# Optimization experiments

Hardware: AMD Instinct MI355X
Metric: run time of the kernel (lower is better)

The kernel has to match this reference:

```python
import jax, jax.numpy as jnp
import numpy as np

N = 100000   # nodes
E = 640000   # edges
D = 128      # in_channels
C = 40       # out_channels (classes)


def setup_inputs() -> dict:
    key = jax.random.key(0)
    ks = jax.random.split(key, 6)
    x = jax.random.normal(ks[0], (N, D), jnp.float32)
    edge_index = jax.random.randint(ks[1], (2, E), 0, N)
    edge_weight = jax.random.uniform(ks[2], (E,), jnp.float32)
    # 8 block convs (4 blocks x 2) stacked, + final conv
    Wb = jax.random.normal(ks[3], (8, D, D), jnp.float32) / np.sqrt(D)
    bb = jnp.zeros((8, D), jnp.float32)
    Wf = jax.random.normal(ks[4], (D, C), jnp.float32) / np.sqrt(D)
    bf = jnp.zeros((C,), jnp.float32)
    return dict(x=x, edge_index=edge_index, edge_weight=edge_weight,
                Wb=Wb, bb=bb, Wf=Wf, bf=bf)


def _gcn(x, W, b, src, dst, w):
    """PyG GCNConv (normalize=True) with self-loops already appended to src/dst/w."""
    n = x.shape[0]
    h = x @ W                                   # [N, out]
    deg = jax.ops.segment_sum(w, dst, num_segments=n)
    dinv = jnp.where(deg > 0, jax.lax.rsqrt(deg), 0.0)
    norm = dinv[src] * w * dinv[dst]            # [E+N]
    out = jax.ops.segment_sum(h[src] * norm[:, None], dst, num_segments=n)
    return out + b


def reference(x, edge_index, edge_weight, Wb, bb, Wf, bf):
    n = x.shape[0]
    loop = jnp.arange(n)
    src = jnp.concatenate([edge_index[0], loop])
    dst = jnp.concatenate([edge_index[1], loop])
    w = jnp.concatenate([edge_weight, jnp.ones((n,), x.dtype)])
    # forward only runs blocks 1-4 (blocks 5-7 unused in the original forward)
    for i in range(4):
        identity = x
        x = jax.nn.relu(_gcn(x, Wb[2 * i], bb[2 * i], src, dst, w))
        # dropout: identity in eval mode
        x = jax.nn.relu(_gcn(x, Wb[2 * i + 1], bb[2 * i + 1], src, dst, w))
        # F.normalize: row-wise L2 with eps=1e-12
        x = x / jnp.maximum(jnp.linalg.norm(x, axis=1, keepdims=True), 1e-12)
        x = (x + identity) / 2
    x = _gcn(x, Wf, bf, src, dst, w)
    return jax.nn.log_softmax(x, axis=1)
```

## Files before the change

kernel.cpp:

```cpp
#include <hip/hip_runtime.h>
#include <math.h>

#define NN 100000
#define EE 640000
#define DD 128
#define CC 40
#define FIXS 4194304.0f

typedef __bf16 bf16x8 __attribute__((ext_vector_type(8)));
typedef float f32x4 __attribute__((ext_vector_type(4)));
typedef unsigned short us8 __attribute__((ext_vector_type(8)));

__device__ inline unsigned short f2b(float f) {
    union { float f; unsigned u; } v; v.f = f;
    unsigned u = v.u;
    return (unsigned short)((u + 0x7FFFu + ((u >> 16) & 1u)) >> 16);
}
__device__ inline float b2f(unsigned short b) {
    union { unsigned u; float f; } v; v.u = ((unsigned)b) << 16;
    return v.f;
}


__global__ __launch_bounds__(256) void k_edge1(const int* __restrict__ dst,
                                               const float* __restrict__ w,
                                               unsigned long long* __restrict__ degcnt,
                                               int* __restrict__ pos) {
    int e = blockIdx.x * 256 + threadIdx.x;
    if (e < EE) {
        int d = dst[e];
        unsigned long long pk =
            ((unsigned long long)(unsigned)(w[e] * FIXS) << 32) | 1ull;
        unsigned long long old = atomicAdd(&degcnt[d], pk);
        pos[e] = (int)(old & 0xffffffffull);
    }
}

__global__ __launch_bounds__(256) void k_scan1p(const unsigned long long* __restrict__ degcnt,
                                                float* __restrict__ dinv,
                                                int* __restrict__ out,
                                                int* __restrict__ partial,
                                                const float* __restrict__ Wb,
                                                const float* __restrict__ Wf,
                                                unsigned short* __restrict__ WT,
                                                unsigned short* __restrict__ WfT) {
    int t = threadIdx.x;
    if (blockIdx.x >= 98) {
        int idx = (blockIdx.x - 98) * 256 + t;
        if (idx < 8 * DD * DD) {
            int m = idx >> 14;
            int n = (idx >> 7) & 127;
            int k = idx & 127;
            WT[idx] = f2b(Wb[(size_t)m * DD * DD + (size_t)k * DD + n]);
        } else {
            int j = idx - 8 * DD * DD;
            if (j < 64 * DD) {
                int n = j >> 7;
                int k = j & 127;
                WfT[j] = (n < CC) ? f2b(Wf[(size_t)k * CC + n]) : 0;
            }
        }
        return;
    }
    __shared__ int lds[256];
    int base = blockIdx.x * 1024 + t * 4;
    int v[4]; int s = 0;
    #pragma unroll
    for (int j = 0; j < 4; ++j) {
        int idx = base + j;
        unsigned long long dc = (idx < NN) ? degcnt[idx] : 0ull;
        v[j] = (int)(dc & 0xffffffffull);
        s += v[j];
        if (idx < NN)
            dinv[idx] = rsqrtf((float)(unsigned)(dc >> 32) * (1.0f / FIXS) + 1.0f);
    }
    lds[t] = s;
    __syncthreads();
    for (int off = 1; off < 256; off <<= 1) {
        int x = lds[t];
        int y = (t >= off) ? lds[t - off] : 0;
        __syncthreads();
        lds[t] = x + y;
        __syncthreads();
    }
    int excl = lds[t] - s;
    if (t == 255) partial[blockIdx.x] = lds[255];
    int run = excl;
    #pragma unroll
    for (int j = 0; j < 4; ++j) {
        int idx = base + j;
        if (idx < NN) out[idx] = run;
        run += v[j];
    }
}

__global__ __launch_bounds__(128) void k_scan2(int* __restrict__ partial) {
    __shared__ int lds[128];
    int t = threadIdx.x;
    int v = (t < 98) ? partial[t] : 0;
    lds[t] = v;
    __syncthreads();
    for (int off = 1; off < 128; off <<= 1) {
        int x = lds[t];
        int y = (t >= off) ? lds[t - off] : 0;
        __syncthreads();
        lds[t] = x + y;
        __syncthreads();
    }
    if (t < 98) partial[t] = lds[t] - v;
}

__global__ __launch_bounds__(256) void k_scan3(int* __restrict__ rp,
                                               const int* __restrict__ partial) {
    int i = blockIdx.x * 256 + threadIdx.x;
    if (i < NN) rp[i] += partial[i >> 10];
    if (i == 0) rp[NN] = EE;
}

__global__ __launch_bounds__(256) void k_scatter(const int* __restrict__ src,
                                                 const int* __restrict__ dst,
                                                 const float* __restrict__ w,
                                                 const float* __restrict__ dinv,
                                                 const int* __restrict__ rp,
                                                 const int* __restrict__ pos,
                                                 int* __restrict__ col,
                                                 float* __restrict__ val) {
    int e = blockIdx.x * 256 + threadIdx.x;
    if (e < EE) {
        int s = src[e], d = dst[e];
        int p = rp[d] + pos[e];
        col[p] = s;
        val[p] = dinv[s] * w[e] * dinv[d];
    }
}

__global__ __launch_bounds__(256) void k_x2bf(const float* __restrict__ x,
                                              unsigned short* __restrict__ Abf) {
    int idx = blockIdx.x * 256 + threadIdx.x;
    if (idx >= NN * DD / 4) return;
    float4 v = ((const float4*)x)[idx];
    ushort4 r;
    r.x = f2b(v.x); r.y = f2b(v.y); r.z = f2b(v.z); r.w = f2b(v.w);
    ((ushort4*)Abf)[idx] = r;
}

__global__ __launch_bounds__(256) void k_mm_mfma(const unsigned short* __restrict__ X,
                                                 const unsigned short* __restrict__ WT,
                                                 unsigned short* __restrict__ H) {
    int wid = threadIdx.x >> 6;
    int lane = threadIdx.x & 63;
    int r0 = blockIdx.x * 64 + wid * 16;
    int sl = lane & 15, g = lane >> 4;
    int arow = r0 + sl;
    if (arow >= NN) arow = NN - 1;

    f32x4 acc[8];
    #pragma unroll
    for (int n = 0; n < 8; ++n) acc[n] = (f32x4){0.f, 0.f, 0.f, 0.f};

    const bf16x8* xrow = (const bf16x8*)(X + (size_t)arow * DD);
    #pragma unroll
    for (int kc = 0; kc < 4; ++kc) {
        bf16x8 a = xrow[kc * 4 + g];
        #pragma unroll
        for (int n = 0; n < 8; ++n) {
            const bf16x8* wrow = (const bf16x8*)(WT + (size_t)(n * 16 + sl) * DD);
            bf16x8 b = wrow[kc * 4 + g];
            acc[n] = __builtin_amdgcn_mfma_f32_16x16x32_bf16(a, b, acc[n], 0, 0, 0);
        }
    }
    #pragma unroll
    for (int n = 0; n < 8; ++n) {
        #pragma unroll
        for (int v = 0; v < 4; ++v) {
            int row = r0 + g * 4 + v;
            if (row < NN) H[(size_t)row * DD + n * 16 + sl] = f2b(acc[n][v]);
        }
    }
}

__global__ __launch_bounds__(256) void k_mm40b(const unsigned short* __restrict__ X,
                                               const unsigned short* __restrict__ WfT,
                                               unsigned short* __restrict__ H) {
    int wid = threadIdx.x >> 6;
    int lane = threadIdx.x & 63;
    int r0 = blockIdx.x * 64 + wid * 16;
    int sl = lane & 15, g = lane >> 4;
    int arow = r0 + sl;
    if (arow >= NN) arow = NN - 1;

    f32x4 acc[4];
    #pragma unroll
    for (int n = 0; n < 4; ++n) acc[n] = (f32x4){0.f, 0.f, 0.f, 0.f};

    const bf16x8* xrow = (const bf16x8*)(X + (size_t)arow * DD);
    #pragma unroll
    for (int kc = 0; kc < 4; ++kc) {
        bf16x8 a = xrow[kc * 4 + g];
        #pragma unroll
        for (int n = 0; n < 4; ++n) {
            const bf16x8* wrow = (const bf16x8*)(WfT + (size_t)(n * 16 + sl) * DD);
            bf16x8 b = wrow[kc * 4 + g];
            acc[n] = __builtin_amdgcn_mfma_f32_16x16x32_bf16(a, b, acc[n], 0, 0, 0);
        }
    }
    #pragma unroll
    for (int n = 0; n < 4; ++n) {
        #pragma unroll
        for (int v = 0; v < 4; ++v) {
            int row = r0 + g * 4 + v;
            if (row < NN) H[(size_t)row * 64 + n * 16 + sl] = f2b(acc[n][v]);
        }
    }
}


#define AGG_CORE(h_, node_, sl_, a_, STRIDE_)                               \
    {                                                                       \
        float dv = dinv[node_];                                             \
        float dv2 = dv * dv;                                                \
        us8 m_ = ((const us8*)(h_ + (size_t)node_ * STRIDE_))[sl_];         \
        _Pragma("unroll")                                                   \
        for (int j = 0; j < 8; ++j) a_[j] = dv2 * b2f(m_[j]);               \
        int e = rp[node_], end = rp[node_ + 1];                             \
        for (; e + 4 <= end; e += 4) {                                      \
            int s0 = col[e], s1 = col[e + 1], s2 = col[e + 2], s3 = col[e + 3]; \
            float v0 = val[e], v1 = val[e + 1], v2 = val[e + 2], v3 = val[e + 3]; \
            us8 q0 = ((const us8*)(h_ + (size_t)s0 * STRIDE_))[sl_];        \
            us8 q1 = ((const us8*)(h_ + (size_t)s1 * STRIDE_))[sl_];        \
            us8 q2 = ((const us8*)(h_ + (size_t)s2 * STRIDE_))[sl_];        \
            us8 q3 = ((const us8*)(h_ + (size_t)s3 * STRIDE_))[sl_];        \
            _Pragma("unroll")                                               \
            for (int j = 0; j < 8; ++j)                                     \
                a_[j] += (v0 * b2f(q0[j]) + v1 * b2f(q1[j]))                \
                       + (v2 * b2f(q2[j]) + v3 * b2f(q3[j]));               \
        }                                                                   \
        for (; e < end; ++e) {                                              \
            int s0 = col[e];                                                \
            float v0 = val[e];                                              \
            us8 q0 = ((const us8*)(h_ + (size_t)s0 * STRIDE_))[sl_];        \
            _Pragma("unroll")                                               \
            for (int j = 0; j < 8; ++j) a_[j] += v0 * b2f(q0[j]);           \
        }                                                                   \
    }

__global__ __launch_bounds__(256) void k_agg128(const unsigned short* __restrict__ h,
                                                const float* __restrict__ dinv,
                                                const int* __restrict__ rp,
                                                const int* __restrict__ col,
                                                const float* __restrict__ val,
                                                const float* __restrict__ bias,
                                                unsigned short* __restrict__ outb) {
    int node = blockIdx.x * 16 + (threadIdx.x >> 4);
    int sl = threadIdx.x & 15;
    if (node >= NN) return;
    float a[8];
    AGG_CORE(h, node, sl, a, DD);
    float4 bz0 = ((const float4*)bias)[sl * 2];
    float4 bz1 = ((const float4*)bias)[sl * 2 + 1];
    float bb[8] = {bz0.x, bz0.y, bz0.z, bz0.w, bz1.x, bz1.y, bz1.z, bz1.w};
    us8 r;
    #pragma unroll
    for (int j = 0; j < 8; ++j) r[j] = f2b(fmaxf(a[j] + bb[j], 0.f));
    ((us8*)(outb + (size_t)node * DD))[sl] = r;
}

__global__ __launch_bounds__(256) void k_agg128_nr(const unsigned short* __restrict__ h,
                                                   const float* __restrict__ dinv,
                                                   const int* __restrict__ rp,
                                                   const int* __restrict__ col,
                                                   const float* __restrict__ val,
                                                   const float* __restrict__ bias,
                                                   unsigned short* __restrict__ Abf) {
    int node = blockIdx.x * 16 + (threadIdx.x >> 4);
    int sl = threadIdx.x & 15;
    if (node >= NN) return;
    float a[8];
    AGG_CORE(h, node, sl, a, DD);
    float4 bz0 = ((const float4*)bias)[sl * 2];
    float4 bz1 = ((const float4*)bias)[sl * 2 + 1];
    float bb[8] = {bz0.x, bz0.y, bz0.z, bz0.w, bz1.x, bz1.y, bz1.z, bz1.w};
    float ss = 0.f;
    #pragma unroll
    for (int j = 0; j < 8; ++j) {
        a[j] = fmaxf(a[j] + bb[j], 0.f);
        ss += a[j] * a[j];
    }
    ss += __shfl_xor(ss, 1);
    ss += __shfl_xor(ss, 2);
    ss += __shfl_xor(ss, 4);
    ss += __shfl_xor(ss, 8);
    float sc = 1.0f / fmaxf(sqrtf(ss), 1e-12f);
    us8 oldb = ((const us8*)(Abf + (size_t)node * DD))[sl];
    us8 rb;
    #pragma unroll
    for (int j = 0; j < 8; ++j)
        rb[j] = f2b((a[j] * sc + b2f(oldb[j])) * 0.5f);
    ((us8*)(Abf + (size_t)node * DD))[sl] = rb;
}

__global__ __launch_bounds__(256) void k_agg_final(const unsigned short* __restrict__ h,
                                                   const float* __restrict__ dinv,
                                                   const int* __restrict__ rp,
                                                   const int* __restrict__ col,
                                                   const float* __restrict__ val,
                                                   const float* __restrict__ bias,
                                                   float* __restrict__ out) {
    int node = blockIdx.x * 32 + (threadIdx.x >> 3);
    int sl = threadIdx.x & 7;
    if (node >= NN) return;
    float a[8];
    AGG_CORE(h, node, sl, a, 64);
    bool real = sl < 5;
    float vv[8];
    if (real) {
        float4 bz0 = ((const float4*)bias)[sl * 2];
        float4 bz1 = ((const float4*)bias)[sl * 2 + 1];
        float bb[8] = {bz0.x, bz0.y, bz0.z, bz0.w, bz1.x, bz1.y, bz1.z, bz1.w};
        #pragma unroll
        for (int j = 0; j < 8; ++j) vv[j] = a[j] + bb[j];
    } else {
        #pragma unroll
        for (int j = 0; j < 8; ++j) vv[j] = -3.0e38f;
    }
    float m = vv[0];
    #pragma unroll
    for (int j = 1; j < 8; ++j) m = fmaxf(m, vv[j]);
    m = fmaxf(m, __shfl_xor(m, 1));
    m = fmaxf(m, __shfl_xor(m, 2));
    m = fmaxf(m, __shfl_xor(m, 4));
    float s = 0.f;
    if (real) {
        #pragma unroll
        for (int j = 0; j < 8; ++j) s += expf(vv[j] - m);
    }
    s += __shfl_xor(s, 1);
    s += __shfl_xor(s, 2);
    s += __shfl_xor(s, 4);
    float ls = m + logf(s);
    if (real) {
        float4 o0 = {vv[0] - ls, vv[1] - ls, vv[2] - ls, vv[3] - ls};
        float4 o1 = {vv[4] - ls, vv[5] - ls, vv[6] - ls, vv[7] - ls};
        float* orow = out + (size_t)node * CC + sl * 8;
        *(float4*)(orow) = o0;
        *(float4*)(orow + 4) = o1;
    }
}


extern "C" void kernel_launch(void* const* d_in, const int* in_sizes, int n_in,
                              void* d_out, int out_size, void* d_ws, size_t ws_size,
                              hipStream_t stream) {
    const float* x  = (const float*)d_in[0];
    const int*   ei = (const int*)d_in[1];
    const float* ew = (const float*)d_in[2];
    const float* Wb = (const float*)d_in[3];
    const float* bb = (const float*)d_in[4];
    const float* Wf = (const float*)d_in[5];
    const float* bf_ = (const float*)d_in[6];
    const int* src = ei;
    const int* dst = ei + EE;
    float* out = (float*)d_out;

    char* p = (char*)d_ws;
    unsigned short*     Abf    = (unsigned short*)p;     p += (size_t)NN * DD * 2;
    unsigned short*     Bbf    = (unsigned short*)p;     p += (size_t)NN * DD * 2;
    unsigned short*     Cbf    = (unsigned short*)p;     p += (size_t)NN * DD * 2;
    unsigned short*     H48    = (unsigned short*)p;     p += (size_t)NN * 64 * 2;
    unsigned short*     WT     = (unsigned short*)p;     p += (size_t)8 * DD * DD * 2;
    unsigned short*     WfT    = (unsigned short*)p;     p += (size_t)64 * DD * 2;
    unsigned long long* degcnt = (unsigned long long*)p; p += (size_t)NN * 8;
    float* dinv = (float*)p; p += (size_t)NN * 4;
    int*   rp   = (int*)p;   p += (size_t)(NN + 1) * 4;
    int*   pos  = (int*)p;   p += (size_t)EE * 4;
    int*   col  = (int*)p;   p += (size_t)EE * 4;
    float* val  = (float*)p; p += (size_t)EE * 4;
    int*   partial = (int*)p; p += 128 * 4;

    hipMemsetAsync(degcnt, 0, (size_t)NN * 8, stream);

    k_edge1<<<(EE + 255) / 256, 256, 0, stream>>>(dst, ew, degcnt, pos);
    k_scan1p<<<98 + (8 * DD * DD + 64 * DD + 255) / 256, 256, 0, stream>>>(
        degcnt, dinv, rp, partial, Wb, Wf, WT, WfT);
    k_scan2<<<1, 128, 0, stream>>>(partial);
    k_scan3<<<(NN + 255) / 256, 256, 0, stream>>>(rp, partial);
    k_scatter<<<(EE + 255) / 256, 256, 0, stream>>>(src, dst, ew, dinv, rp, pos, col, val);
    k_x2bf<<<(NN * DD / 4 + 255) / 256, 256, 0, stream>>>(x, Abf);

    int gb = (NN + 63) / 64;
    for (int blk = 0; blk < 4; ++blk) {
        k_mm_mfma<<<gb, 256, 0, stream>>>(Abf, WT + (size_t)(2 * blk) * DD * DD, Bbf);
        k_agg128<<<(NN + 15) / 16, 256, 0, stream>>>(Bbf, dinv, rp, col, val,
                                                     bb + (size_t)(2 * blk) * DD, Cbf);
        k_mm_mfma<<<gb, 256, 0, stream>>>(Cbf, WT + (size_t)(2 * blk + 1) * DD * DD, Bbf);
        k_agg128_nr<<<(NN + 15) / 16, 256, 0, stream>>>(Bbf, dinv, rp, col, val,
                                                        bb + (size_t)(2 * blk + 1) * DD, Abf);
    }
    k_mm40b<<<gb, 256, 0, stream>>>(Abf, WfT, H48);
    k_agg_final<<<(NN + 31) / 32, 256, 0, stream>>>(H48, dinv, rp, col, val, bf_, out);
}
```

Before: 661.3 us.

## Interleave CSR col/val, fuse scan and x-conversion, stage GEMM output via LDS

Packs CSR column index and edge norm into one int2 array, so each aggregation edge needs one 8-byte load instead of two separate loads. Merges the single-block partial scan into k_scan3 (every block redoes the 98-entry scan in LDS), and folds the fp32-to-bf16 input conversion into the first GEMM so the separate x2bf pass over x is removed. The MFMA GEMM epilogue now goes through an LDS tile, giving 16-byte coalesced row stores instead of scattered 2-byte stores. The costs are extra LDS use and a __syncthreads in the GEMMs, plus redundant scan work in each k_scan3 block.

```diff
diff --git a/kernel.cpp b/kernel.cpp
--- a/kernel.cpp
+++ b/kernel.cpp
@@ -94,26 +94,25 @@
     }
 }
 
-__global__ __launch_bounds__(128) void k_scan2(int* __restrict__ partial) {
+__global__ __launch_bounds__(256) void k_scan3(int* __restrict__ rp,
+                                               const int* __restrict__ partial) {
     __shared__ int lds[128];
     int t = threadIdx.x;
-    int v = (t < 98) ? partial[t] : 0;
-    lds[t] = v;
+    if (t < 128) lds[t] = (t < 98) ? partial[t] : 0;
     __syncthreads();
     for (int off = 1; off < 128; off <<= 1) {
-        int x = lds[t];
-        int y = (t >= off) ? lds[t - off] : 0;
+        int x = (t < 128) ? lds[t] : 0;
+        int y = (t >= off && t < 128) ? lds[t - off] : 0;
         __syncthreads();
-        lds[t] = x + y;
+        if (t < 128) lds[t] = x + y;
         __syncthreads();
     }
-    if (t < 98) partial[t] = lds[t] - v;
-}
-
-__global__ __launch_bounds__(256) void k_scan3(int* __restrict__ rp,
-                                               const int* __restrict__ partial) {
-    int i = blockIdx.x * 256 + threadIdx.x;
-    if (i < NN) rp[i] += partial[i >> 10];
+    int i = blockIdx.x * 256 + t;
+    if (i < NN) {
+        int c = i >> 10;
+        int add = c ? lds[c - 1] : 0;
+        rp[i] += add;
+    }
     if (i == 0) rp[NN] = EE;
 }
 
@@ -123,30 +122,81 @@
                                                  const float* __restrict__ dinv,
                                                  const int* __restrict__ rp,
                                                  const int* __restrict__ pos,
-                                                 int* __restrict__ col,
-                                                 float* __restrict__ val) {
+                                                 int2* __restrict__ cvp) {
     int e = blockIdx.x * 256 + threadIdx.x;
     if (e < EE) {
         int s = src[e], d = dst[e];
         int p = rp[d] + pos[e];
-        col[p] = s;
-        val[p] = dinv[s] * w[e] * dinv[d];
-    }
-}
-
-__global__ __launch_bounds__(256) void k_x2bf(const float* __restrict__ x,
-                                              unsigned short* __restrict__ Abf) {
-    int idx = blockIdx.x * 256 + threadIdx.x;
-    if (idx >= NN * DD / 4) return;
-    float4 v = ((const float4*)x)[idx];
-    ushort4 r;
-    r.x = f2b(v.x); r.y = f2b(v.y); r.z = f2b(v.z); r.w = f2b(v.w);
-    ((ushort4*)Abf)[idx] = r;
+        int2 cv;
+        cv.x = s;
+        cv.y = __float_as_int(dinv[s] * w[e] * dinv[d]);
+        cvp[p] = cv;
+    }
+}
+
+
+#define MM_EPILOGUE_128(H_)                                                  \
+    {                                                                        \
+        _Pragma("unroll")                                                    \
+        for (int n = 0; n < 8; ++n) {                                        \
+            _Pragma("unroll")                                                \
+            for (int v = 0; v < 4; ++v)                                      \
+                tb[wid][g * 4 + v][n * 16 + sl] = f2b(acc[n][v]);            \
+        }                                                                    \
+        __syncthreads();                                                     \
+        _Pragma("unroll")                                                    \
+        for (int c4 = 0; c4 < 4; ++c4) {                                     \
+            int chunk = c4 * 64 + lane;                                      \
+            int row = chunk >> 4, seg = chunk & 15;                          \
+            int grow = r0 + row;                                             \
+            if (grow < NN)                                                   \
+                *(us8*)(H_ + (size_t)grow * DD + seg * 8) =                  \
+                    *(const us8*)(&tb[wid][row][seg * 8]);                   \
+        }                                                                    \
+    }
+
+__global__ __launch_bounds__(256) void k_mmx(const float* __restrict__ x,
+                                             const unsigned short* __restrict__ WT,
+                                             unsigned short* __restrict__ Abf,
+                                             unsigned short* __restrict__ H) {
+    __shared__ unsigned short tb[4][16][136];
+    int wid = threadIdx.x >> 6;
+    int lane = threadIdx.x & 63;
+    int r0 = blockIdx.x * 64 + wid * 16;
+    int sl = lane & 15, g = lane >> 4;
+    int arow = r0 + sl;
+    bool avalid = arow < NN;
+    if (!avalid) arow = NN - 1;
+
+    f32x4 acc[8];
+    #pragma unroll
+    for (int n = 0; n < 8; ++n) acc[n] = (f32x4){0.f, 0.f, 0.f, 0.f};
+
+    const float* xrow = x + (size_t)arow * DD;
+    #pragma unroll
+    for (int kc = 0; kc < 4; ++kc) {
+        int chunk = kc * 4 + g;
+        float4 lo = *(const float4*)(xrow + chunk * 8);
+        float4 hi = *(const float4*)(xrow + chunk * 8 + 4);
+        us8 r;
+        r[0] = f2b(lo.x); r[1] = f2b(lo.y); r[2] = f2b(lo.z); r[3] = f2b(lo.w);
+        r[4] = f2b(hi.x); r[5] = f2b(hi.y); r[6] = f2b(hi.z); r[7] = f2b(hi.w);
+        if (avalid) ((us8*)(Abf + (size_t)arow * DD))[chunk] = r;
+        bf16x8 a = *(bf16x8*)&r;
+        #pragma unroll
+        for (int n = 0; n < 8; ++n) {
+            const bf16x8* wrow = (const bf16x8*)(WT + (size_t)(n * 16 + sl) * DD);
+            bf16x8 b = wrow[kc * 4 + g];
+            acc[n] = __builtin_amdgcn_mfma_f32_16x16x32_bf16(a, b, acc[n], 0, 0, 0);
+        }
+    }
+    MM_EPILOGUE_128(H);
 }
 
 __global__ __launch_bounds__(256) void k_mm_mfma(const unsigned short* __restrict__ X,
                                                  const unsigned short* __restrict__ WT,
                                                  unsigned short* __restrict__ H) {
+    __shared__ unsigned short tb[4][16][136];
     int wid = threadIdx.x >> 6;
     int lane = threadIdx.x & 63;
     int r0 = blockIdx.x * 64 + wid * 16;
@@ -169,14 +219,7 @@
             acc[n] = __builtin_amdgcn_mfma_f32_16x16x32_bf16(a, b, acc[n], 0, 0, 0);
         }
     }
-    #pragma unroll
-    for (int n = 0; n < 8; ++n) {
-        #pragma unroll
-        for (int v = 0; v < 4; ++v) {
-            int row = r0 + g * 4 + v;
-            if (row < NN) H[(size_t)row * DD + n * 16 + sl] = f2b(acc[n][v]);
-        }
-    }
+    MM_EPILOGUE_128(H);
 }
 
 __global__ __launch_bounds__(256) void k_mm40b(const unsigned short* __restrict__ X,
@@ -224,21 +267,22 @@
         for (int j = 0; j < 8; ++j) a_[j] = dv2 * b2f(m_[j]);               \
         int e = rp[node_], end = rp[node_ + 1];                             \
         for (; e + 4 <= end; e += 4) {                                      \
-            int s0 = col[e], s1 = col[e + 1], s2 = col[e + 2], s3 = col[e + 3]; \
-            float v0 = val[e], v1 = val[e + 1], v2 = val[e + 2], v3 = val[e + 3]; \
-            us8 q0 = ((const us8*)(h_ + (size_t)s0 * STRIDE_))[sl_];        \
-            us8 q1 = ((const us8*)(h_ + (size_t)s1 * STRIDE_))[sl_];        \
-            us8 q2 = ((const us8*)(h_ + (size_t)s2 * STRIDE_))[sl_];        \
-            us8 q3 = ((const us8*)(h_ + (size_t)s3 * STRIDE_))[sl_];        \
+            int2 c0 = cvp[e], c1 = cvp[e + 1], c2 = cvp[e + 2], c3 = cvp[e + 3]; \
+            us8 q0 = ((const us8*)(h_ + (size_t)c0.x * STRIDE_))[sl_];      \
+            us8 q1 = ((const us8*)(h_ + (size_t)c1.x * STRIDE_))[sl_];      \
+            us8 q2 = ((const us8*)(h_ + (size_t)c2.x * STRIDE_))[sl_];      \
+            us8 q3 = ((const us8*)(h_ + (size_t)c3.x * STRIDE_))[sl_];      \
+            float v0 = __int_as_float(c0.y), v1 = __int_as_float(c1.y);     \
+            float v2 = __int_as_float(c2.y), v3 = __int_as_float(c3.y);     \
             _Pragma("unroll")                                               \
             for (int j = 0; j < 8; ++j)                                     \
                 a_[j] += (v0 * b2f(q0[j]) + v1 * b2f(q1[j]))                \
                        + (v2 * b2f(q2[j]) + v3 * b2f(q3[j]));               \
         }                                                                   \
         for (; e < end; ++e) {                                              \
-            int s0 = col[e];                                                \
-            float v0 = val[e];                                              \
-            us8 q0 = ((const us8*)(h_ + (size_t)s0 * STRIDE_))[sl_];        \
+            int2 c0 = cvp[e];                                               \
+            us8 q0 = ((const us8*)(h_ + (size_t)c0.x * STRIDE_))[sl_];      \
+            float v0 = __int_as_float(c0.y);                                \
             _Pragma("unroll")                                               \
             for (int j = 0; j < 8; ++j) a_[j] += v0 * b2f(q0[j]);           \
         }                                                                   \
@@ -247,8 +291,7 @@
 __global__ __launch_bounds__(256) void k_agg128(const unsigned short* __restrict__ h,
                                                 const float* __restrict__ dinv,
                                                 const int* __restrict__ rp,
-                                                const int* __restrict__ col,
-                                                const float* __restrict__ val,
+                                                const int2* __restrict__ cvp,
                                                 const float* __restrict__ bias,
                                                 unsigned short* __restrict__ outb) {
     int node = blockIdx.x * 16 + (threadIdx.x >> 4);
@@ -268,8 +311,7 @@
 __global__ __launch_bounds__(256) void k_agg128_nr(const unsigned short* __restrict__ h,
                                                    const float* __restrict__ dinv,
                                                    const int* __restrict__ rp,
-                                                   const int* __restrict__ col,
-                                                   const float* __restrict__ val,
+                                                   const int2* __restrict__ cvp,
                                                    const float* __restrict__ bias,
                                                    unsigned short* __restrict__ Abf) {
     int node = blockIdx.x * 16 + (threadIdx.x >> 4);
@@ -302,8 +344,7 @@
 __global__ __launch_bounds__(256) void k_agg_final(const unsigned short* __restrict__ h,
                                                    const float* __restrict__ dinv,
                                                    const int* __restrict__ rp,
-                                                   const int* __restrict__ col,
-                                                   const float* __restrict__ val,
+                                                   const int2* __restrict__ cvp,
                                                    const float* __restrict__ bias,
                                                    float* __restrict__ out) {
     int node = blockIdx.x * 32 + (threadIdx.x >> 3);
@@ -373,8 +414,7 @@
     float* dinv = (float*)p; p += (size_t)NN * 4;
     int*   rp   = (int*)p;   p += (size_t)(NN + 1) * 4;
     int*   pos  = (int*)p;   p += (size_t)EE * 4;
-    int*   col  = (int*)p;   p += (size_t)EE * 4;
-    float* val  = (float*)p; p += (size_t)EE * 4;
+    int2*  cvp  = (int2*)p;  p += (size_t)EE * 8;
     int*   partial = (int*)p; p += 128 * 4;
 
     hipMemsetAsync(degcnt, 0, (size_t)NN * 8, stream);
@@ -382,20 +422,20 @@
     k_edge1<<<(EE + 255) / 256, 256, 0, stream>>>(dst, ew, degcnt, pos);
     k_scan1p<<<98 + (8 * DD * DD + 64 * DD + 255) / 256, 256, 0, stream>>>(
         degcnt, dinv, rp, partial, Wb, Wf, WT, WfT);
-    k_scan2<<<1, 128, 0, stream>>>(partial);
     k_scan3<<<(NN + 255) / 256, 256, 0, stream>>>(rp, partial);
-    k_scatter<<<(EE + 255) / 256, 256, 0, stream>>>(src, dst, ew, dinv, rp, pos, col, val);
-    k_x2bf<<<(NN * DD / 4 + 255) / 256, 256, 0, stream>>>(x, Abf);
+    k_scatter<<<(EE + 255) / 256, 256, 0, stream>>>(src, dst, ew, dinv, rp, pos, cvp);
 
     int gb = (NN + 63) / 64;
+    k_mmx<<<gb, 256, 0, stream>>>(x, WT, Abf, Bbf);
     for (int blk = 0; blk < 4; ++blk) {
-        k_mm_mfma<<<gb, 256, 0, stream>>>(Abf, WT + (size_t)(2 * blk) * DD * DD, Bbf);
-        k_agg128<<<(NN + 15) / 16, 256, 0, stream>>>(Bbf, dinv, rp, col, val,
+        k_agg128<<<(NN + 15) / 16, 256, 0, stream>>>(Bbf, dinv, rp, cvp,
                                                      bb + (size_t)(2 * blk) * DD, Cbf);
         k_mm_mfma<<<gb, 256, 0, stream>>>(Cbf, WT + (size_t)(2 * blk + 1) * DD * DD, Bbf);
-        k_agg128_nr<<<(NN + 15) / 16, 256, 0, stream>>>(Bbf, dinv, rp, col, val,
+        k_agg128_nr<<<(NN + 15) / 16, 256, 0, stream>>>(Bbf, dinv, rp, cvp,
                                                         bb + (size_t)(2 * blk + 1) * DD, Abf);
+        if (blk < 3)
+            k_mm_mfma<<<gb, 256, 0, stream>>>(Abf, WT + (size_t)(2 * blk + 2) * DD * DD, Bbf);
     }
     k_mm40b<<<gb, 256, 0, stream>>>(Abf, WfT, H48);
-    k_agg_final<<<(NN + 31) / 32, 256, 0, stream>>>(H48, dinv, rp, col, val, bf_, out);
-}
+    k_agg_final<<<(NN + 31) / 32, 256, 0, stream>>>(H48, dinv, rp, cvp, bf_, out);
+}
```

Measured after the change: 637.0 us, median of 2. 1.04x faster.
